# Performance work log

Measured on AMD Instinct MI355X. Metric: run time of the kernel, lower is better.

The kernel has to match this reference:

```python
import jax, jax.numpy as jnp
import numpy as np

B, H, S, D = 2, 16, 2048, 128


def setup_inputs() -> dict:
    key = jax.random.key(0)
    kq, kk, kv = jax.random.split(key, 3)
    q = jax.random.normal(kq, (B, H, S, D), dtype=jnp.float32)
    k = jax.random.normal(kk, (B, H, S, D), dtype=jnp.float32)
    v = jax.random.normal(kv, (B, H, S, D), dtype=jnp.float32)
    return {"q": q, "k": k, "v": v}


def reference(q, k, v):
    # cp_size == 1 path: causal scaled dot-product attention.
    # Identical math to the ring online-softmax accumulation collapsed to one step.
    d = q.shape[-1]
    scale = d ** -0.5
    scores = jnp.einsum("bhsd,bhtd->bhst", q, k) * scale  # (B,H,S,S)
    s = scores.shape[-1]
    causal_mask = jnp.tril(jnp.ones((s, s), dtype=bool))  # (S,S)
    scores = jnp.where(causal_mask, scores, -jnp.inf)
    probs = jax.nn.softmax(scores, axis=-1)
    return jnp.einsum("bhst,bhtd->bhsd", probs, v)
```

## Files before the change

### kernel.cpp

```cpp
#include <hip/hip_runtime.h>
#include <hip/hip_bf16.h>

constexpr int Bb = 2, Hh = 16, Ss = 2048, Dd = 128;
constexpr int BM = 64, BN = 64;
constexpr int NQT = Ss / BM;
constexpr float SCALE = 0.088388347648318447f;

typedef __attribute__((ext_vector_type(8))) short bf16x8;
typedef __attribute__((ext_vector_type(4))) float f32x4;
typedef __attribute__((ext_vector_type(4))) int int4v;

__device__ __forceinline__ unsigned bfbits(float f) {
  union { float f; unsigned u; } v; v.f = f;
  return v.u + 0x7FFFu + ((v.u >> 16) & 1u);
}
__device__ __forceinline__ short f2bf(float f) { return (short)(bfbits(f) >> 16); }
__device__ __forceinline__ unsigned packbf(float lo, float hi) {
  return (bfbits(lo) >> 16) | (bfbits(hi) & 0xFFFF0000u);
}
__device__ __forceinline__ float fcomp(float4 f, int j) {
  return j == 0 ? f.x : (j == 1 ? f.y : (j == 2 ? f.z : f.w));
}

__global__ __launch_bounds__(256, 2)
void fa_fwd_kernel(const float* __restrict__ q, const float* __restrict__ k,
                   const float* __restrict__ v, float* __restrict__ out) {
  __shared__ __align__(16) char Klds[BN * 256];
  __shared__ __align__(16) char Vlds[Dd * 128];

  const int tid = threadIdx.x;
  const int wave = tid >> 6, lane = tid & 63, quad = lane >> 4, l16 = lane & 15;
  const int bid = blockIdx.x;
  const int bh = bid & 31;
  const int qt = (NQT - 1) - (bid >> 5);

  const float* qb = q + (size_t)bh * Ss * Dd;
  const float* kb = k + (size_t)bh * Ss * Dd;
  const float* vb = v + (size_t)bh * Ss * Dd;

  bf16x8 qf[4];
  {
    const float* qr = qb + (size_t)(qt * BM + wave * 16 + l16) * Dd + quad * 8;
    #pragma unroll
    for (int ks = 0; ks < 4; ++ks) {
      float4 a = *(const float4*)(qr + ks * 32);
      float4 b = *(const float4*)(qr + ks * 32 + 4);
      bf16x8 t;
      t[0]=f2bf(a.x*SCALE); t[1]=f2bf(a.y*SCALE); t[2]=f2bf(a.z*SCALE); t[3]=f2bf(a.w*SCALE);
      t[4]=f2bf(b.x*SCALE); t[5]=f2bf(b.y*SCALE); t[6]=f2bf(b.z*SCALE); t[7]=f2bf(b.w*SCALE);
      qf[ks] = t;
    }
  }

  const int krow0 = tid >> 4;
  const int kblk  = tid & 15;
  const int kswz  = kblk ^ krow0;
  const int vkg = tid >> 5;
  const int vdq = tid & 31;

  float4 ka[4], kc[4];
  float4 vr[8];

  auto load_tiles = [&](int kt) {
    const float* Kg = kb + (size_t)(kt * BN) * Dd + kblk * 8;
    #pragma unroll
    for (int i = 0; i < 4; ++i) {
      ka[i] = *(const float4*)(Kg + (size_t)(krow0 + 16 * i) * Dd);
      kc[i] = *(const float4*)(Kg + (size_t)(krow0 + 16 * i) * Dd + 4);
    }
    const float* Vg = vb + (size_t)(kt * BN + vkg * 8) * Dd + vdq * 4;
    #pragma unroll
    for (int r = 0; r < 8; ++r)
      vr[r] = *(const float4*)(Vg + (size_t)r * Dd);
  };

  auto stage_tiles = [&]() {
    #pragma unroll
    for (int i = 0; i < 4; ++i) {
      bf16x8 t;
      t[0]=f2bf(ka[i].x); t[1]=f2bf(ka[i].y); t[2]=f2bf(ka[i].z); t[3]=f2bf(ka[i].w);
      t[4]=f2bf(kc[i].x); t[5]=f2bf(kc[i].y); t[6]=f2bf(kc[i].z); t[7]=f2bf(kc[i].w);
      *(bf16x8*)(Klds + (krow0 + 16 * i) * 256 + kswz * 16) = t;
    }
    #pragma unroll
    for (int j = 0; j < 4; ++j) {
      int d = vdq * 4 + j;
      int f7 = (d ^ (d >> 3)) & 7;
      bf16x8 t;
      #pragma unroll
      for (int r = 0; r < 8; ++r) t[r] = f2bf(fcomp(vr[r], j));
      *(bf16x8*)(Vlds + d * 128 + (vkg ^ f7) * 16) = t;
    }
  };

  f32x4 o[8];
  #pragma unroll
  for (int i = 0; i < 8; ++i) o[i] = (f32x4)(0.0f);
  float mrow = -3.0e38f, lrow = 0.0f;

  load_tiles(0);
  stage_tiles();

  const int hi2 = quad >> 1;
  const int srcbase = (l16 + 32 * (quad & 1)) * 4;

  for (int kt = 0; kt <= qt; ++kt) {
    __syncthreads();
    const bool more = kt < qt;
    if (more) load_tiles(kt + 1);

    f32x4 acc[4];
    #pragma unroll
    for (int nt = 0; nt < 4; ++nt) acc[nt] = (f32x4)(0.0f);
    #pragma unroll
    for (int ks = 0; ks < 4; ++ks) {
      #pragma unroll
      for (int nt = 0; nt < 4; ++nt) {
        int row = nt * 16 + l16;
        int bswz = (ks * 4 + quad) ^ l16;
        bf16x8 kf = *(const bf16x8*)(Klds + row * 256 + bswz * 16);
        acc[nt] = __builtin_amdgcn_mfma_f32_16x16x32_bf16(kf, qf[ks], acc[nt], 0, 0, 0);
      }
    }

    if (kt == qt) {
      #pragma unroll
      for (int nt = 0; nt < 4; ++nt)
        #pragma unroll
        for (int r = 0; r < 4; ++r)
          if (nt * 16 + quad * 4 + r > wave * 16 + l16) acc[nt][r] = -1.0e30f;
    }

    float mx = acc[0][0];
    #pragma unroll
    for (int nt = 0; nt < 4; ++nt)
      #pragma unroll
      for (int r = 0; r < 4; ++r) mx = fmaxf(mx, acc[nt][r]);
    mx = fmaxf(mx, __shfl_xor(mx, 16, 64));
    mx = fmaxf(mx, __shfl_xor(mx, 32, 64));
    float mn = fmaxf(mrow, mx);
    float alpha = __expf(mrow - mn);
    mrow = mn;
    float rs = 0.f;
    #pragma unroll
    for (int nt = 0; nt < 4; ++nt)
      #pragma unroll
      for (int r = 0; r < 4; ++r) {
        float p = __expf(acc[nt][r] - mn);
        acc[nt][r] = p; rs += p;
      }
    rs += __shfl_xor(rs, 16, 64);
    rs += __shfl_xor(rs, 32, 64);
    lrow = lrow * alpha + rs;

    unsigned pk0_0 = packbf(acc[0][0], acc[0][1]), pk0_1 = packbf(acc[0][2], acc[0][3]);
    unsigned pk1_0 = packbf(acc[1][0], acc[1][1]), pk1_1 = packbf(acc[1][2], acc[1][3]);
    unsigned pk2_0 = packbf(acc[2][0], acc[2][1]), pk2_1 = packbf(acc[2][2], acc[2][3]);
    unsigned pk3_0 = packbf(acc[3][0], acc[3][1]), pk3_1 = packbf(acc[3][2], acc[3][3]);

    #pragma unroll
    for (int r = 0; r < 4; ++r) {
      int src = (lane & 48) | (quad * 4 + r);
      float ar = __shfl(alpha, src, 64);
      #pragma unroll
      for (int dt = 0; dt < 8; ++dt) o[dt][r] *= ar;
    }

    bf16x8 pf[2];
    {
      int4v p0, p1;
      #pragma unroll
      for (int jp = 0; jp < 4; ++jp) {
        int srcb = srcbase + 64 * (jp >> 1);
        int a0 = __builtin_amdgcn_ds_bpermute(srcb, (int)((jp & 1) ? pk0_1 : pk0_0));
        int a1 = __builtin_amdgcn_ds_bpermute(srcb, (int)((jp & 1) ? pk1_1 : pk1_0));
        int a2 = __builtin_amdgcn_ds_bpermute(srcb, (int)((jp & 1) ? pk2_1 : pk2_0));
        int a3 = __builtin_amdgcn_ds_bpermute(srcb, (int)((jp & 1) ? pk3_1 : pk3_0));
        p0[jp] = hi2 ? a1 : a0;
        p1[jp] = hi2 ? a3 : a2;
      }
      pf[0] = __builtin_bit_cast(bf16x8, p0);
      pf[1] = __builtin_bit_cast(bf16x8, p1);
    }

    #pragma unroll
    for (int ks2 = 0; ks2 < 2; ++ks2) {
      #pragma unroll
      for (int dt = 0; dt < 8; ++dt) {
        int row = dt * 16 + l16;
        int f7 = (row ^ (row >> 3)) & 7;
        int bswz = (ks2 * 4 + quad) ^ f7;
        bf16x8 vf = *(const bf16x8*)(Vlds + row * 128 + bswz * 16);
        o[dt] = __builtin_amdgcn_mfma_f32_16x16x32_bf16(pf[ks2], vf, o[dt], 0, 0, 0);
      }
    }

    if (more) { __syncthreads(); stage_tiles(); }
  }

  float linv[4];
  #pragma unroll
  for (int r = 0; r < 4; ++r) {
    int src = (lane & 48) | (quad * 4 + r);
    linv[r] = 1.0f / __shfl(lrow, src, 64);
  }
  float* ob = out + ((size_t)bh * Ss + qt * BM + wave * 16) * Dd;
  #pragma unroll
  for (int dt = 0; dt < 8; ++dt)
    #pragma unroll
    for (int r = 0; r < 4; ++r)
      ob[(quad * 4 + r) * Dd + dt * 16 + l16] = o[dt][r] * linv[r];
}

extern "C" void kernel_launch(void* const* d_in, const int* in_sizes, int n_in,
                              void* d_out, int out_size, void* d_ws, size_t ws_size,
                              hipStream_t stream) {
  const float* q = (const float*)d_in[0];
  const float* k = (const float*)d_in[1];
  const float* v = (const float*)d_in[2];
  float* out = (float*)d_out;
  dim3 grid(Bb * Hh * NQT);
  dim3 block(256);
  hipLaunchKernelGGL(fa_fwd_kernel, grid, block, 0, stream, q, k, v, out);
}
```

Baseline: 202.7 us.

## Use hardware bf16 packing, exp2 softmax, lazy rescale, deferred row-sum reduction, setprio

```diff
diff --git a/kernel.cpp b/kernel.cpp
--- a/kernel.cpp
+++ b/kernel.cpp
@@ -4,19 +4,21 @@
 constexpr int Bb = 2, Hh = 16, Ss = 2048, Dd = 128;
 constexpr int BM = 64, BN = 64;
 constexpr int NQT = Ss / BM;
-constexpr float SCALE = 0.088388347648318447f;
+constexpr float SCALE = 0.088388347648318447f * 1.4426950408889634f;
 
 typedef __attribute__((ext_vector_type(8))) short bf16x8;
 typedef __attribute__((ext_vector_type(4))) float f32x4;
 typedef __attribute__((ext_vector_type(4))) int int4v;
 
-__device__ __forceinline__ unsigned bfbits(float f) {
-  union { float f; unsigned u; } v; v.f = f;
-  return v.u + 0x7FFFu + ((v.u >> 16) & 1u);
-}
-__device__ __forceinline__ short f2bf(float f) { return (short)(bfbits(f) >> 16); }
-__device__ __forceinline__ unsigned packbf(float lo, float hi) {
-  return (bfbits(lo) >> 16) | (bfbits(hi) & 0xFFFF0000u);
+__device__ __forceinline__ unsigned cvtpk(float lo, float hi) {
+  unsigned r;
+  asm("v_cvt_pk_bf16_f32 %0, %1, %2" : "=v"(r) : "v"(lo), "v"(hi));
+  return r;
+}
+__device__ __forceinline__ float exp2hw(float x) {
+  float r;
+  asm("v_exp_f32 %0, %1" : "=v"(r) : "v"(x));
+  return r;
 }
 __device__ __forceinline__ float fcomp(float4 f, int j) {
   return j == 0 ? f.x : (j == 1 ? f.y : (j == 2 ? f.z : f.w));
@@ -45,10 +47,12 @@
     for (int ks = 0; ks < 4; ++ks) {
       float4 a = *(const float4*)(qr + ks * 32);
       float4 b = *(const float4*)(qr + ks * 32 + 4);
-      bf16x8 t;
-      t[0]=f2bf(a.x*SCALE); t[1]=f2bf(a.y*SCALE); t[2]=f2bf(a.z*SCALE); t[3]=f2bf(a.w*SCALE);
-      t[4]=f2bf(b.x*SCALE); t[5]=f2bf(b.y*SCALE); t[6]=f2bf(b.z*SCALE); t[7]=f2bf(b.w*SCALE);
-      qf[ks] = t;
+      int4v t;
+      t[0] = (int)cvtpk(a.x * SCALE, a.y * SCALE);
+      t[1] = (int)cvtpk(a.z * SCALE, a.w * SCALE);
+      t[2] = (int)cvtpk(b.x * SCALE, b.y * SCALE);
+      t[3] = (int)cvtpk(b.z * SCALE, b.w * SCALE);
+      qf[ks] = __builtin_bit_cast(bf16x8, t);
     }
   }
 
@@ -77,19 +81,23 @@
   auto stage_tiles = [&]() {
     #pragma unroll
     for (int i = 0; i < 4; ++i) {
-      bf16x8 t;
-      t[0]=f2bf(ka[i].x); t[1]=f2bf(ka[i].y); t[2]=f2bf(ka[i].z); t[3]=f2bf(ka[i].w);
-      t[4]=f2bf(kc[i].x); t[5]=f2bf(kc[i].y); t[6]=f2bf(kc[i].z); t[7]=f2bf(kc[i].w);
-      *(bf16x8*)(Klds + (krow0 + 16 * i) * 256 + kswz * 16) = t;
+      int4v t;
+      t[0] = (int)cvtpk(ka[i].x, ka[i].y);
+      t[1] = (int)cvtpk(ka[i].z, ka[i].w);
+      t[2] = (int)cvtpk(kc[i].x, kc[i].y);
+      t[3] = (int)cvtpk(kc[i].z, kc[i].w);
+      *(int4v*)(Klds + (krow0 + 16 * i) * 256 + kswz * 16) = t;
     }
     #pragma unroll
     for (int j = 0; j < 4; ++j) {
       int d = vdq * 4 + j;
       int f7 = (d ^ (d >> 3)) & 7;
-      bf16x8 t;
-      #pragma unroll
-      for (int r = 0; r < 8; ++r) t[r] = f2bf(fcomp(vr[r], j));
-      *(bf16x8*)(Vlds + d * 128 + (vkg ^ f7) * 16) = t;
+      int4v t;
+      t[0] = (int)cvtpk(fcomp(vr[0], j), fcomp(vr[1], j));
+      t[1] = (int)cvtpk(fcomp(vr[2], j), fcomp(vr[3], j));
+      t[2] = (int)cvtpk(fcomp(vr[4], j), fcomp(vr[5], j));
+      t[3] = (int)cvtpk(fcomp(vr[6], j), fcomp(vr[7], j));
+      *(int4v*)(Vlds + d * 128 + (vkg ^ f7) * 16) = t;
     }
   };
 
@@ -112,6 +120,7 @@
     f32x4 acc[4];
     #pragma unroll
     for (int nt = 0; nt < 4; ++nt) acc[nt] = (f32x4)(0.0f);
+    __builtin_amdgcn_s_setprio(1);
     #pragma unroll
     for (int ks = 0; ks < 4; ++ks) {
       #pragma unroll
@@ -122,6 +131,7 @@
         acc[nt] = __builtin_amdgcn_mfma_f32_16x16x32_bf16(kf, qf[ks], acc[nt], 0, 0, 0);
       }
     }
+    __builtin_amdgcn_s_setprio(0);
 
     if (kt == qt) {
       #pragma unroll
@@ -138,33 +148,35 @@
       for (int r = 0; r < 4; ++r) mx = fmaxf(mx, acc[nt][r]);
     mx = fmaxf(mx, __shfl_xor(mx, 16, 64));
     mx = fmaxf(mx, __shfl_xor(mx, 32, 64));
-    float mn = fmaxf(mrow, mx);
-    float alpha = __expf(mrow - mn);
-    mrow = mn;
+
+    if (!__all(mx - mrow <= 8.0f)) {
+      float mn = fmaxf(mrow, mx);
+      float alpha = exp2hw(mrow - mn);
+      mrow = mn;
+      lrow *= alpha;
+      #pragma unroll
+      for (int r = 0; r < 4; ++r) {
+        int src = (lane & 48) | (quad * 4 + r);
+        float ar = __shfl(alpha, src, 64);
+        #pragma unroll
+        for (int dt = 0; dt < 8; ++dt) o[dt][r] *= ar;
+      }
+    }
+
     float rs = 0.f;
     #pragma unroll
     for (int nt = 0; nt < 4; ++nt)
       #pragma unroll
       for (int r = 0; r < 4; ++r) {
-        float p = __expf(acc[nt][r] - mn);
+        float p = exp2hw(acc[nt][r] - mrow);
         acc[nt][r] = p; rs += p;
       }
-    rs += __shfl_xor(rs, 16, 64);
-    rs += __shfl_xor(rs, 32, 64);
-    lrow = lrow * alpha + rs;
-
-    unsigned pk0_0 = packbf(acc[0][0], acc[0][1]), pk0_1 = packbf(acc[0][2], acc[0][3]);
-    unsigned pk1_0 = packbf(acc[1][0], acc[1][1]), pk1_1 = packbf(acc[1][2], acc[1][3]);
-    unsigned pk2_0 = packbf(acc[2][0], acc[2][1]), pk2_1 = packbf(acc[2][2], acc[2][3]);
-    unsigned pk3_0 = packbf(acc[3][0], acc[3][1]), pk3_1 = packbf(acc[3][2], acc[3][3]);
-
-    #pragma unroll
-    for (int r = 0; r < 4; ++r) {
-      int src = (lane & 48) | (quad * 4 + r);
-      float ar = __shfl(alpha, src, 64);
-      #pragma unroll
-      for (int dt = 0; dt < 8; ++dt) o[dt][r] *= ar;
-    }
+    lrow += rs;
+
+    unsigned pk0_0 = cvtpk(acc[0][0], acc[0][1]), pk0_1 = cvtpk(acc[0][2], acc[0][3]);
+    unsigned pk1_0 = cvtpk(acc[1][0], acc[1][1]), pk1_1 = cvtpk(acc[1][2], acc[1][3]);
+    unsigned pk2_0 = cvtpk(acc[2][0], acc[2][1]), pk2_1 = cvtpk(acc[2][2], acc[2][3]);
+    unsigned pk3_0 = cvtpk(acc[3][0], acc[3][1]), pk3_1 = cvtpk(acc[3][2], acc[3][3]);
 
     bf16x8 pf[2];
     {
@@ -183,6 +195,7 @@
       pf[1] = __builtin_bit_cast(bf16x8, p1);
     }
 
+    __builtin_amdgcn_s_setprio(1);
     #pragma unroll
     for (int ks2 = 0; ks2 < 2; ++ks2) {
       #pragma unroll
@@ -194,10 +207,13 @@
         o[dt] = __builtin_amdgcn_mfma_f32_16x16x32_bf16(pf[ks2], vf, o[dt], 0, 0, 0);
       }
     }
+    __builtin_amdgcn_s_setprio(0);
 
     if (more) { __syncthreads(); stage_tiles(); }
   }
 
+  lrow += __shfl_xor(lrow, 16, 64);
+  lrow += __shfl_xor(lrow, 32, 64);
   float linv[4];
   #pragma unroll
   for (int r = 0; r < 4; ++r) {
```

Result: faster. 189.2 us (-6.6%).
